# Kernel optimization log

Hardware: AMD Instinct MI355X
Metric: run time of the kernel (lower is better)

The kernel has to match this reference:

```python
import jax, jax.numpy as jnp
import numpy as np

BS, NQ, D, NH, NP, L, DFF = 4, 1024, 256, 8, 4, 6, 1024
H_BEV, W_BEV = 200, 150
NV = H_BEV * W_BEV
DH = D // NH


def setup_inputs() -> dict:
    key = jax.random.key(0)
    ks = iter(jax.random.split(key, 64))
    r = lambda *s: jax.random.normal(next(ks), s, dtype=jnp.float32)
    return {
        'query': r(BS, NQ, D),
        'query_pos': r(BS, NQ, D),
        'reference_points': jax.random.uniform(next(ks), (BS, NQ, 1, 2), dtype=jnp.float32),
        'src': r(BS, NV, D),
        'spatial_shapes': jnp.array([[H_BEV, W_BEV]], dtype=jnp.int32),
        'level_start_index': jnp.array([0], dtype=jnp.int32),
        'sa_in_w': r(L, 3 * D, D) * 0.02, 'sa_in_b': jnp.zeros((L, 3 * D), jnp.float32),
        'sa_out_w': r(L, D, D) * 0.02, 'sa_out_b': jnp.zeros((L, D), jnp.float32),
        'ca_off_w': r(L, NH * NP * 2, D) * 0.01, 'ca_off_b': r(L, NH * NP * 2) * 0.5,
        'ca_aw_w': r(L, NH * NP, D) * 0.01, 'ca_aw_b': jnp.zeros((L, NH * NP), jnp.float32),
        'ca_val_w': r(L, D, D) * 0.02, 'ca_val_b': jnp.zeros((L, D), jnp.float32),
        'ca_out_w': r(L, D, D) * 0.02, 'ca_out_b': jnp.zeros((L, D), jnp.float32),
        'n1_w': jnp.ones((L, D), jnp.float32), 'n1_b': jnp.zeros((L, D), jnp.float32),
        'n2_w': jnp.ones((L, D), jnp.float32), 'n2_b': jnp.zeros((L, D), jnp.float32),
        'n3_w': jnp.ones((L, D), jnp.float32), 'n3_b': jnp.zeros((L, D), jnp.float32),
        'ff1_w': r(L, DFF, D) * 0.02, 'ff1_b': jnp.zeros((L, DFF), jnp.float32),
        'ff2_w': r(L, D, DFF) * 0.02, 'ff2_b': jnp.zeros((L, D), jnp.float32),
    }


def layer_norm(x, w, b, eps=1e-5):
    m = jnp.mean(x, -1, keepdims=True)
    v = jnp.mean(jnp.square(x - m), -1, keepdims=True)
    return (x - m) / jnp.sqrt(v + eps) * w + b


def mha_self(x_qk, x_v, in_w, in_b, out_w, out_b):
    bs, nq, d = x_qk.shape
    qw, kw, vw = jnp.split(in_w, 3, axis=0)
    qb, kb, vb = jnp.split(in_b, 3, axis=0)
    q = (x_qk @ qw.T + qb).reshape(bs, nq, NH, DH)
    k = (x_qk @ kw.T + kb).reshape(bs, nq, NH, DH)
    v = (x_v @ vw.T + vb).reshape(bs, nq, NH, DH)
    att = jax.nn.softmax(jnp.einsum('bqhd,bkhd->bhqk', q, k) / jnp.sqrt(jnp.float32(DH)), axis=-1)
    o = jnp.einsum('bhqk,bkhd->bqhd', att, v).reshape(bs, nq, d)
    return o @ out_w.T + out_b


def msda(q, ref, src, lsi0, off_w, off_b, aw_w, aw_b, val_w, val_b, out_w, out_b):
    # single-level (n_levels=1) multi-scale deformable attention, grid_sample
    # bilinear with align_corners=False and zero padding, as in mmcv.
    bs, nq, d = q.shape
    v = (src @ val_w.T + val_b).reshape(bs, NV, NH, DH)
    vt = v.transpose(0, 2, 1, 3)  # (bs, NH, NV, DH)
    off = (q @ off_w.T + off_b).reshape(bs, nq, NH, NP, 2)
    aw = jax.nn.softmax((q @ aw_w.T + aw_b).reshape(bs, nq, NH, NP), axis=-1)
    norm = jnp.array([W_BEV, H_BEV], dtype=q.dtype)  # offset_normalizer = (W, H)
    loc = ref[:, :, None, 0, None, :] + off / norm  # (bs, nq, NH, NP, 2) in [0,1]
    x = loc[..., 0] * W_BEV - 0.5
    y = loc[..., 1] * H_BEV - 0.5
    x0 = jnp.floor(x)
    y0 = jnp.floor(y)
    acc = jnp.zeros((bs, NH, nq, NP, DH), q.dtype)
    for dx, dy in ((0, 0), (1, 0), (0, 1), (1, 1)):
        xi = x0 + dx
        yi = y0 + dy
        w = (1.0 - jnp.abs(x - xi)) * (1.0 - jnp.abs(y - yi))
        valid = (xi >= 0) & (xi < W_BEV) & (yi >= 0) & (yi < H_BEV)
        w = jnp.where(valid, w, 0.0)  # (bs, nq, NH, NP)
        xi_c = jnp.clip(xi, 0, W_BEV - 1).astype(jnp.int32)
        yi_c = jnp.clip(yi, 0, H_BEV - 1).astype(jnp.int32)
        idx = lsi0 + yi_c * W_BEV + xi_c  # flat index into NV
        idx_t = idx.transpose(0, 2, 1, 3).reshape(bs, NH, nq * NP)
        g = jnp.take_along_axis(vt, idx_t[..., None], axis=2).reshape(bs, NH, nq, NP, DH)
        acc = acc + g * w.transpose(0, 2, 1, 3)[..., None]
    o = jnp.einsum('bhqpd,bqhp->bqhd', acc, aw).reshape(bs, nq, d)
    return o @ out_w.T + out_b


def _forward(query, query_pos, reference_points, src,
             sa_in_w, sa_in_b, sa_out_w, sa_out_b,
             ca_off_w, ca_off_b, ca_aw_w, ca_aw_b, ca_val_w, ca_val_b, ca_out_w, ca_out_b,
             n1_w, n1_b, n2_w, n2_b, n3_w, n3_b,
             ff1_w, ff1_b, ff2_w, ff2_b,
             spatial_shapes, level_start_index):
    lsi0 = level_start_index[0]
    out = query
    inter = []
    for l in range(L):
        qk = out + query_pos
        sa = mha_self(qk, out, sa_in_w[l], sa_in_b[l], sa_out_w[l], sa_out_b[l])
        out = layer_norm(out + sa, n2_w[l], n2_b[l])
        ca = msda(out + query_pos, reference_points, src, lsi0,
                  ca_off_w[l], ca_off_b[l], ca_aw_w[l], ca_aw_b[l],
                  ca_val_w[l], ca_val_b[l], ca_out_w[l], ca_out_b[l])
        out = layer_norm(out + ca, n1_w[l], n1_b[l])
        ff = jax.nn.relu(out @ ff1_w[l].T + ff1_b[l]) @ ff2_w[l].T + ff2_b[l]
        out = layer_norm(out + ff, n3_w[l], n3_b[l])
        inter.append(out)
    hs = jnp.stack(inter)  # (L, bs, nq, D)
    refs = jnp.stack([reference_points] * L)  # (L, bs, nq, 1, 2)
    return hs, refs


def reference(query, query_pos, reference_points, src, spatial_shapes, level_start_index,
              sa_in_w, sa_in_b, sa_out_w, sa_out_b,
              ca_off_w, ca_off_b, ca_aw_w, ca_aw_b, ca_val_w, ca_val_b, ca_out_w, ca_out_b,
              n1_w, n1_b, n2_w, n2_b, n3_w, n3_b,
              ff1_w, ff1_b, ff2_w, ff2_b):
    return _forward(query, query_pos, reference_points, src,
                    sa_in_w, sa_in_b, sa_out_w, sa_out_b,
                    ca_off_w, ca_off_b, ca_aw_w, ca_aw_b, ca_val_w, ca_val_b, ca_out_w, ca_out_b,
                    n1_w, n1_b, n2_w, n2_b, n3_w, n3_b,
                    ff1_w, ff1_b, ff2_w, ff2_b,
                    spatial_shapes, level_start_index)
```

## Files before the change

### kernel.cpp

```cpp
#include <hip/hip_runtime.h>

typedef __attribute__((ext_vector_type(8))) short short8;
typedef __attribute__((ext_vector_type(4))) short short4v;
typedef __attribute__((ext_vector_type(4))) float f32x4;
typedef unsigned short u16;

#define DEVI static __device__ __forceinline__

DEVI float b2f(u16 u){ unsigned int x = ((unsigned int)u) << 16; float f; __builtin_memcpy(&f, &x, 4); return f; }
DEVI u16 f2b(float f){ unsigned int u; __builtin_memcpy(&u, &f, 4); u += 0x7fffu + ((u >> 16) & 1u); return (u16)(u >> 16); }
DEVI short8 cvt8(const float* __restrict__ p){
  f32x4 a = *(const f32x4*)p;
  f32x4 b = *(const f32x4*)(p + 4);
  short8 r;
  r[0]=(short)f2b(a[0]); r[1]=(short)f2b(a[1]); r[2]=(short)f2b(a[2]); r[3]=(short)f2b(a[3]);
  r[4]=(short)f2b(b[0]); r[5]=(short)f2b(b[1]); r[6]=(short)f2b(b[2]); r[7]=(short)f2b(b[3]);
  return r;
}

__global__ __launch_bounds__(256) void cvt_k(const float* __restrict__ s, u16* __restrict__ d, int n8){
  int i = blockIdx.x * 256 + threadIdx.x;
  if (i < n8) ((short8*)d)[i] = cvt8(s + (long)i * 8);
}

__global__ __launch_bounds__(256) void offaw_pack_k(
    const float* __restrict__ off_w, const float* __restrict__ aw_w,
    const float* __restrict__ off_b, const float* __restrict__ aw_b,
    u16* __restrict__ wofaw, float* __restrict__ obc)
{
  int tid = blockIdx.x * 256 + threadIdx.x;
  if (tid < 98304) {
    int l = tid / 16384, rem = tid - l * 16384;
    wofaw[l * 24576 + rem] = f2b(off_w[tid]);
  } else if (tid < 147456) {
    int t2 = tid - 98304;
    int l = t2 / 8192, rem = t2 - l * 8192;
    wofaw[l * 24576 + 16384 + rem] = f2b(aw_w[t2]);
  } else if (tid < 147840) {
    int t3 = tid - 147456;
    obc[(t3 / 64) * 96 + (t3 % 64)] = off_b[t3];
  } else if (tid < 148032) {
    int t4 = tid - 147840;
    obc[(t4 / 32) * 96 + 64 + (t4 % 32)] = aw_b[t4];
  }
}

__global__ __launch_bounds__(256) void flash_k(
    const u16* __restrict__ qkbuf, const u16* __restrict__ vt,
    u16* __restrict__ obuf)
{
  const float SC = 0.17677669529663687f;
  __shared__ u16 Plds[4][32][136];
  const int bh = blockIdx.x >> 3;
  const int b = bh >> 3, h = bh & 7;
  const int qt = blockIdx.x & 7;
  const int wave = threadIdx.x >> 6, lane = threadIdx.x & 63;
  const int lr = lane & 15, lq = lane >> 4;
  const int qbase = qt * 128 + wave * 32;

  short8 qf[2];
#pragma unroll
  for (int i = 0; i < 2; i++)
    qf[i] = *(const short8*)(qkbuf + (long)(b * 1024 + qbase + i * 16 + lr) * 512 + h * 32 + lq * 8);

  const u16* Kb = qkbuf + (long)b * 1024 * 512 + 256 + h * 32;
  const u16* Vb = vt + (long)bh * 32 * 1024;

  f32x4 acc_o[2][2] = {};
  float m_run[2][4], l_run[2][4];
#pragma unroll
  for (int i = 0; i < 2; i++)
#pragma unroll
    for (int r = 0; r < 4; r++){ m_run[i][r] = -3e38f; l_run[i][r] = 0.f; }

  for (int kt = 0; kt < 8; kt++) {
    f32x4 s[2][8] = {};
#pragma unroll
    for (int j = 0; j < 8; j++) {
      short8 kf = *(const short8*)(Kb + (long)(kt * 128 + j * 16 + lr) * 512 + lq * 8);
#pragma unroll
      for (int i = 0; i < 2; i++)
        s[i][j] = __builtin_amdgcn_mfma_f32_16x16x32_bf16(qf[i], kf, s[i][j], 0, 0, 0);
    }
#pragma unroll
    for (int i = 0; i < 2; i++) {
#pragma unroll
      for (int r = 0; r < 4; r++) {
        float mx = s[i][0][r];
#pragma unroll
        for (int j = 1; j < 8; j++) mx = fmaxf(mx, s[i][j][r]);
#pragma unroll
        for (int m = 1; m <= 8; m <<= 1) mx = fmaxf(mx, __shfl_xor(mx, m));
        float m_new = fmaxf(m_run[i][r], mx);
        float alpha = __expf((m_run[i][r] - m_new) * SC);
        float sum = 0.f;
        int row = i * 16 + lq * 4 + r;
#pragma unroll
        for (int j = 0; j < 8; j++) {
          float p = __expf((s[i][j][r] - m_new) * SC);
          sum += p;
          Plds[wave][row][j * 16 + lr] = f2b(p);
        }
#pragma unroll
        for (int m = 1; m <= 8; m <<= 1) sum += __shfl_xor(sum, m);
        l_run[i][r] = l_run[i][r] * alpha + sum;
        m_run[i][r] = m_new;
#pragma unroll
        for (int d = 0; d < 2; d++) acc_o[i][d][r] *= alpha;
      }
    }
#pragma unroll
    for (int kc = 0; kc < 4; kc++) {
      short8 pf[2];
#pragma unroll
      for (int i = 0; i < 2; i++)
        pf[i] = *(const short8*)&Plds[wave][i * 16 + lr][kc * 32 + lq * 8];
#pragma unroll
      for (int d = 0; d < 2; d++) {
        short8 vf = *(const short8*)(Vb + (long)(d * 16 + lr) * 1024 + kt * 128 + kc * 32 + lq * 8);
#pragma unroll
        for (int i = 0; i < 2; i++)
          acc_o[i][d] = __builtin_amdgcn_mfma_f32_16x16x32_bf16(pf[i], vf, acc_o[i][d], 0, 0, 0);
      }
    }
  }
#pragma unroll
  for (int i = 0; i < 2; i++) {
#pragma unroll
    for (int r = 0; r < 4; r++) {
      float inv = 1.f / l_run[i][r];
      int q = qbase + i * 16 + lq * 4 + r;
#pragma unroll
      for (int d = 0; d < 2; d++)
        obuf[(long)(b * 1024 + q) * 256 + h * 32 + d * 16 + lr] = f2b(acc_o[i][d][r] * inv);
    }
  }
}

template<bool RELU, bool OUTBF, bool VT, bool LN>
__global__ __launch_bounds__(256) void gemm_w_k(
    const u16* __restrict__ A, int lda,
    const u16* __restrict__ W,
    const float* __restrict__ bias,
    void* __restrict__ Cv, int ldo,
    int M, int N, int K,
    u16* __restrict__ vt,
    const float* __restrict__ res,
    const float* __restrict__ lnw, const float* __restrict__ lnb,
    const float* __restrict__ qpos,
    float* __restrict__ out_f, u16* __restrict__ out_b16,
    u16* __restrict__ qk_b16, float* __restrict__ hsp)
{
  __shared__ u16 As[32][64][8];
  __shared__ float r1s[4][64], r2s[4][64], mArr[64], iArr[64];
  const int wave = threadIdx.x >> 6, lane = threadIdx.x & 63;
  const int bm = blockIdx.x * 64;
  const int bn = blockIdx.y * 256 + wave * 64;
  const int lr = lane & 15, lq = lane >> 4;
  f32x4 acc[4][4] = {};
  const int nchunks = K >> 8;
  for (int ch = 0; ch < nchunks; ch++) {
    const u16* ga = A + (long)(bm + lane) * lda + ch * 256;
#pragma unroll
    for (int g = 0; g < 8; g++) {
      int kgrp = wave * 8 + g;
      __builtin_amdgcn_global_load_lds(
          (const __attribute__((address_space(1))) void*)(ga + kgrp * 8),
          (__attribute__((address_space(3))) void*)&As[kgrp][0][0], 16, 0, 0);
    }
    __syncthreads();
#pragma unroll
    for (int s = 0; s < 8; s++) {
      short8 af[4], bf[4];
#pragma unroll
      for (int i = 0; i < 4; i++)
        af[i] = *(const short8*)&As[s * 4 + lq][i * 16 + lr][0];
#pragma unroll
      for (int j = 0; j < 4; j++) {
        int cc = bn + j * 16 + lr;
        bf[j] = *(const short8*)(W + (long)cc * K + ch * 256 + s * 32 + lq * 8);
      }
#pragma unroll
      for (int i = 0; i < 4; i++)
#pragma unroll
        for (int j = 0; j < 4; j++)
          acc[i][j] = __builtin_amdgcn_mfma_f32_16x16x32_bf16(af[i], bf[j], acc[i][j], 0, 0, 0);
    }
    __syncthreads();
  }

  float bv[4];
#pragma unroll
  for (int j = 0; j < 4; j++) bv[j] = bias[bn + j * 16 + lr];

  if (!LN) {
#pragma unroll
    for (int j = 0; j < 4; j++) {
      int cc = bn + j * 16 + lr;
#pragma unroll
      for (int i = 0; i < 4; i++) {
#pragma unroll
        for (int r = 0; r < 4; r++) {
          int rr = bm + i * 16 + lq * 4 + r;
          float v = acc[i][j][r] + bv[j];
          if (RELU) v = fmaxf(v, 0.f);
          long idx = (long)rr * ldo + cc;
          if (OUTBF) ((u16*)Cv)[idx] = f2b(v);
          else       ((float*)Cv)[idx] = v;
          if (VT) {
            int b_ = rr >> 10, q_ = rr & 1023, h_ = cc >> 5, dh_ = cc & 31;
            vt[(long)((((b_ << 3) + h_) << 5) + dh_) * 1024 + q_] = f2b(v);
          }
        }
      }
    }
  } else {
    float s1[4][4] = {}, s2[4][4] = {};
#pragma unroll
    for (int i = 0; i < 4; i++) {
#pragma unroll
      for (int r = 0; r < 4; r++) {
        int rowg = bm + i * 16 + lq * 4 + r;
#pragma unroll
        for (int j = 0; j < 4; j++) {
          int cc = bn + j * 16 + lr;
          float x = acc[i][j][r] + bv[j] + res[(long)rowg * 256 + cc];
          s1[i][r] += x; s2[i][r] += x * x;
        }
      }
    }
#pragma unroll
    for (int i = 0; i < 4; i++)
#pragma unroll
      for (int r = 0; r < 4; r++) {
#pragma unroll
        for (int m = 1; m <= 8; m <<= 1) {
          s1[i][r] += __shfl_xor(s1[i][r], m);
          s2[i][r] += __shfl_xor(s2[i][r], m);
        }
      }
    if (lr == 0) {
#pragma unroll
      for (int i = 0; i < 4; i++)
#pragma unroll
        for (int r = 0; r < 4; r++) {
          int rl = i * 16 + lq * 4 + r;
          r1s[wave][rl] = s1[i][r];
          r2s[wave][rl] = s2[i][r];
        }
    }
    __syncthreads();
    if (threadIdx.x < 64) {
      int t = threadIdx.x;
      float a = r1s[0][t] + r1s[1][t] + r1s[2][t] + r1s[3][t];
      float b = r2s[0][t] + r2s[1][t] + r2s[2][t] + r2s[3][t];
      float m = a * (1.f / 256.f);
      float var = b * (1.f / 256.f) - m * m;
      mArr[t] = m;
      iArr[t] = rsqrtf(var + 1e-5f);
    }
    __syncthreads();
#pragma unroll
    for (int i = 0; i < 4; i++) {
#pragma unroll
      for (int r = 0; r < 4; r++) {
        int rl = i * 16 + lq * 4 + r;
        int rowg = bm + rl;
        float m = mArr[rl], inv = iArr[rl];
#pragma unroll
        for (int j = 0; j < 4; j++) {
          int cc = bn + j * 16 + lr;
          long idx = (long)rowg * 256 + cc;
          float x = acc[i][j][r] + bv[j] + res[idx];
          float y = (x - m) * inv * lnw[cc] + lnb[cc];
          out_f[idx] = y;
          if (out_b16) out_b16[idx] = f2b(y);
          if (qk_b16)  qk_b16[idx]  = f2b(y + qpos[idx]);
          if (hsp)     hsp[idx]     = y;
        }
      }
    }
  }
}

template<bool ABF, bool WBF, bool BIAS, bool RELU, bool OUTBF>
__global__ __launch_bounds__(256) void gemm64_k(
    const void* __restrict__ Av, int lda, long sA2, long sA1,
    const void* __restrict__ Wv, int ldw, long sW2, long sW1,
    const float* __restrict__ bias,
    void* __restrict__ Cv, int ldo, long sC2, long sC1,
    int M, int N, int K, int zshift)
{
  const int z  = blockIdx.z;
  const int z2 = z >> zshift, z1 = z - (z2 << zshift);
  const long aoff = z2 * sA2 + z1 * sA1;
  const long woff = z2 * sW2 + z1 * sW1;
  const long coff = z2 * sC2 + z1 * sC1;
  const int wave = threadIdx.x >> 6, lane = threadIdx.x & 63;
  const int wm = wave >> 1, wn = wave & 1;
  const int bm = blockIdx.x * 64 + wm * 32;
  const int bn = blockIdx.y * 64 + wn * 32;
  const int lr = lane & 15, lq = lane >> 4;
  const int koff = lq * 8;
  f32x4 acc[2][2] = {};
  const short8 Z8 = {0,0,0,0,0,0,0,0};
  for (int k0 = 0; k0 < K; k0 += 32) {
    short8 af[2], bf[2];
#pragma unroll
    for (int i = 0; i < 2; i++) {
      int r = bm + i * 16 + lr;
      if (r < M) {
        long o = aoff + (long)r * lda + k0 + koff;
        af[i] = ABF ? *(const short8*)((const u16*)Av + o) : cvt8((const float*)Av + o);
      } else af[i] = Z8;
    }
#pragma unroll
    for (int j = 0; j < 2; j++) {
      int c = bn + j * 16 + lr;
      if (c < N) {
        long o = woff + (long)c * ldw + k0 + koff;
        bf[j] = WBF ? *(const short8*)((const u16*)Wv + o) : cvt8((const float*)Wv + o);
      } else bf[j] = Z8;
    }
#pragma unroll
    for (int i = 0; i < 2; i++)
#pragma unroll
      for (int j = 0; j < 2; j++)
        acc[i][j] = __builtin_amdgcn_mfma_f32_16x16x32_bf16(af[i], bf[j], acc[i][j], 0, 0, 0);
  }
#pragma unroll
  for (int j = 0; j < 2; j++) {
    int cc = bn + j * 16 + lr;
    if (cc >= N) continue;
    float bv = BIAS ? bias[cc] : 0.f;
#pragma unroll
    for (int i = 0; i < 2; i++) {
#pragma unroll
      for (int r = 0; r < 4; r++) {
        int rr = bm + i * 16 + lq * 4 + r;
        if (rr >= M) continue;
        float v = acc[i][j][r] + bv;
        if (RELU) v = fmaxf(v, 0.f);
        long idx = coff + (long)rr * ldo + cc;
        if (OUTBF) ((u16*)Cv)[idx] = f2b(v);
        else       ((float*)Cv)[idx] = v;
      }
    }
  }
}

__global__ __launch_bounds__(256) void init_prep_k(const float* __restrict__ q, const float* __restrict__ qpos,
                                                   float* __restrict__ out_f, u16* __restrict__ out_b,
                                                   u16* __restrict__ qk_b){
  long i = (long)blockIdx.x * 256 + threadIdx.x;
  float o = q[i];
  out_f[i] = o;
  out_b[i] = f2b(o);
  qk_b[i]  = f2b(o + qpos[i]);
}

__global__ __launch_bounds__(256) void vt_k(const u16* __restrict__ V, u16* __restrict__ Vt){
  int tid = blockIdx.x * 256 + threadIdx.x;
  int q = tid & 1023;
  int rest = tid >> 10;
  int dh = rest & 31, h = (rest >> 5) & 7, b = rest >> 8;
  Vt[tid] = V[(long)((b << 10) + q) * 256 + (h << 5) + dh];
}

__global__ __launch_bounds__(256) void softmax_k(u16* __restrict__ S, float scale){
  long row = blockIdx.x;
  u16* p = S + row * 1024;
  int t = threadIdx.x;
  short4v sv = *(short4v*)(p + t * 4);
  float v[4]; float mx = -1e30f;
#pragma unroll
  for (int i = 0; i < 4; i++){ v[i] = b2f((u16)sv[i]); mx = fmaxf(mx, v[i]); }
  __shared__ float red[256];
  red[t] = mx; __syncthreads();
  for (int s = 128; s > 0; s >>= 1){ if (t < s) red[t] = fmaxf(red[t], red[t + s]); __syncthreads(); }
  mx = red[0]; __syncthreads();
  float sum = 0.f;
#pragma unroll
  for (int i = 0; i < 4; i++){ v[i] = __expf((v[i] - mx) * scale); sum += v[i]; }
  red[t] = sum; __syncthreads();
  for (int s = 128; s > 0; s >>= 1){ if (t < s) red[t] += red[t + s]; __syncthreads(); }
  float inv = 1.f / red[0];
#pragma unroll
  for (int i = 0; i < 4; i++) sv[i] = (short)f2b(v[i] * inv);
  *(short4v*)(p + t * 4) = sv;
}

template<bool QKPOS, bool HS, bool OUTB>
__global__ __launch_bounds__(256) void add_ln_k(
    const float* __restrict__ sub,
    const float* __restrict__ w, const float* __restrict__ b,
    const float* __restrict__ qpos,
    float* __restrict__ out_f, u16* __restrict__ out_b,
    u16* __restrict__ qk_b, float* __restrict__ hs)
{
  int row = blockIdx.x, t = threadIdx.x;
  long idx = (long)row * 256 + t;
  float x = out_f[idx] + sub[idx];
  __shared__ float r1[256], r2[256];
  r1[t] = x; r2[t] = x * x; __syncthreads();
  for (int s = 128; s > 0; s >>= 1){ if (t < s){ r1[t] += r1[t + s]; r2[t] += r2[t + s]; } __syncthreads(); }
  float m = r1[0] * (1.f / 256.f);
  float var = r2[0] * (1.f / 256.f) - m * m;
  float y = (x - m) * rsqrtf(var + 1e-5f) * w[t] + b[t];
  out_f[idx] = y;
  if (OUTB)  out_b[idx] = f2b(y);
  if (QKPOS) qk_b[idx]  = f2b(y + qpos[idx]);
  if (HS)    hs[idx]    = y;
}

__global__ __launch_bounds__(256) void msda_k(
    const float* __restrict__ refp,
    const float* __restrict__ off, int ldoff,
    const float* __restrict__ aw, int ldaw,
    const u16* __restrict__ v,
    u16* __restrict__ o,
    int bbase, long vstride)
{
  int tid = blockIdx.x * 256 + threadIdx.x;
  int dh = tid & 31;
  int h  = (tid >> 5) & 7;
  int qq = tid >> 8;
  int bq = (bbase << 10) + qq;
  int b  = bq >> 10;
  float rx = refp[bq * 2 + 0];
  float ry = refp[bq * 2 + 1];
  const float* offp = off + (long)bq * ldoff + h * 8;
  const float* awp  = aw  + (long)bq * ldaw + h * 4;
  float a0 = awp[0], a1 = awp[1], a2 = awp[2], a3 = awp[3];
  float am = fmaxf(fmaxf(a0, a1), fmaxf(a2, a3));
  float e[4];
  e[0] = __expf(a0 - am); e[1] = __expf(a1 - am); e[2] = __expf(a2 - am); e[3] = __expf(a3 - am);
  float einv = 1.f / (e[0] + e[1] + e[2] + e[3]);
  const u16* vb = v + b * vstride + h * 32 + dh;
  float accv = 0.f;
#pragma unroll
  for (int pp = 0; pp < 4; pp++){
    float x = rx * 150.f + offp[pp * 2 + 0] - 0.5f;
    float y = ry * 200.f + offp[pp * 2 + 1] - 0.5f;
    float x0 = floorf(x), y0 = floorf(y);
    float s = 0.f;
#pragma unroll
    for (int c = 0; c < 4; c++){
      int dx = c & 1, dy = c >> 1;
      float xi = x0 + dx, yi = y0 + dy;
      float wt = (1.f - fabsf(x - xi)) * (1.f - fabsf(y - yi));
      if (xi >= 0.f && xi < 150.f && yi >= 0.f && yi < 200.f && wt > 0.f) {
        int xc = (int)xi, yc = (int)yi;
        s += wt * b2f(vb[((long)yc * 150 + xc) * 256]);
      }
    }
    accv += e[pp] * einv * s;
  }
  o[(long)bq * 256 + h * 32 + dh] = f2b(accv);
}

__global__ __launch_bounds__(256) void refs_k(const float* __restrict__ r, float* __restrict__ dst){
  int i = blockIdx.x * 256 + threadIdx.x;
  dst[i] = r[i & 8191];
}

static inline void g64(hipStream_t st, int mode,
    const void* A, int lda, long sA2, long sA1,
    const void* W, int ldw, long sW2, long sW1,
    const float* bias, void* C, int ldo, long sC2, long sC1,
    int M, int N, int K, int Z, int zs)
{
  dim3 g((M + 63) / 64, (N + 63) / 64, Z), b(256, 1, 1);
  switch (mode) {
    case 1: gemm64_k<true, true, true, false,false><<<g,b,0,st>>>(A,lda,sA2,sA1,W,ldw,sW2,sW1,bias,C,ldo,sC2,sC1,M,N,K,zs); break;
    case 2: gemm64_k<true, true, false,false,true ><<<g,b,0,st>>>(A,lda,sA2,sA1,W,ldw,sW2,sW1,bias,C,ldo,sC2,sC1,M,N,K,zs); break;
    case 4: gemm64_k<true, false,true, false,true ><<<g,b,0,st>>>(A,lda,sA2,sA1,W,ldw,sW2,sW1,bias,C,ldo,sC2,sC1,M,N,K,zs); break;
    case 5: gemm64_k<true, false,true, false,false><<<g,b,0,st>>>(A,lda,sA2,sA1,W,ldw,sW2,sW1,bias,C,ldo,sC2,sC1,M,N,K,zs); break;
    case 6: gemm64_k<true, false,true, true, true ><<<g,b,0,st>>>(A,lda,sA2,sA1,W,ldw,sW2,sW1,bias,C,ldo,sC2,sC1,M,N,K,zs); break;
    case 7: gemm64_k<false,false,true, false,true ><<<g,b,0,st>>>(A,lda,sA2,sA1,W,ldw,sW2,sW1,bias,C,ldo,sC2,sC1,M,N,K,zs); break;
  }
}

extern "C" void kernel_launch(void* const* d_in, const int* in_sizes, int n_in,
                              void* d_out, int out_size, void* d_ws, size_t ws_size,
                              hipStream_t stream)
{
  (void)in_sizes; (void)n_in; (void)out_size;
  const float* query = (const float*)d_in[0];
  const float* qpos  = (const float*)d_in[1];
  const float* refp  = (const float*)d_in[2];
  const float* src   = (const float*)d_in[3];
  const float* sa_in_w  = (const float*)d_in[6];
  const float* sa_in_b  = (const float*)d_in[7];
  const float* sa_out_w = (const float*)d_in[8];
  const float* sa_out_b = (const float*)d_in[9];
  const float* off_w = (const float*)d_in[10];
  const float* off_b = (const float*)d_in[11];
  const float* aw_w  = (const float*)d_in[12];
  const float* aw_b  = (const float*)d_in[13];
  const float* val_w = (const float*)d_in[14];
  const float* val_b = (const float*)d_in[15];
  const float* cout_w = (const float*)d_in[16];
  const float* cout_b = (const float*)d_in[17];
  const float* n1w = (const float*)d_in[18]; const float* n1b = (const float*)d_in[19];
  const float* n2w = (const float*)d_in[20]; const float* n2b = (const float*)d_in[21];
  const float* n3w = (const float*)d_in[22]; const float* n3b = (const float*)d_in[23];
  const float* ff1w = (const float*)d_in[24]; const float* ff1b = (const float*)d_in[25];
  const float* ff2w = (const float*)d_in[26]; const float* ff2b = (const float*)d_in[27];

  float* hs = (float*)d_out;
  float* refs_out = hs + (long)6 * 4096 * 256;

  char* base = (char*)d_ws;
  float* out_f = (float*)(base);
  float* tmp_f = (float*)(base + (4u << 20));
  u16*   qk_b  = (u16*)  (base + (8u << 20));
  u16*   out_b = (u16*)  (base + (10u << 20));
  char*  rest  =          base + (12u << 20);

  const size_t NEED_A = 170u << 20;
  const bool planA = (ws_size >= NEED_A);

  init_prep_k<<<4096, 256, 0, stream>>>(query, qpos, out_f, out_b, qk_b);

  if (planA) {
    u16* wsa_b  = (u16*)(rest);
    u16* wsao_b = wsa_b  + 1179648;
    u16* wofaw  = wsao_b + 393216;
    u16* wval_b = wofaw  + 147456;
    u16* wcao_b = wval_b + 393216;
    u16* wff1_b = wcao_b + 393216;
    u16* wff2_b = wff1_b + 1572864;
    u16* src_b  = wff2_b + 1572864;
    float* obc  = (float*)(src_b + 30720000);
    char* U = (char*)(obc + 576);
    u16* qkbuf = (u16*)(U);
    u16* vbuf  = (u16*)(U + (4u << 20));
    u16* vt    = (u16*)(U + (6u << 20));
    u16* obuf  = (u16*)(U + (8u << 20));
    float* oawo = (float*)(U);
    u16*   mo   = (u16*)  (U + (2u << 20));
    u16*   vsrc = (u16*)  (U + (4u << 20));
    u16*   ffh  = (u16*)(U);

    auto cv = [&](const float* s, u16* d, long nel){
      int n8 = (int)(nel / 8);
      cvt_k<<<(n8 + 255) / 256, 256, 0, stream>>>(s, d, n8);
    };
    cv(sa_in_w,  wsa_b,  1179648); cv(sa_out_w, wsao_b, 393216);
    cv(val_w,    wval_b, 393216);  cv(cout_w,   wcao_b, 393216);
    cv(ff1w,     wff1_b, 1572864); cv(ff2w,     wff2_b, 1572864);
    cv(src,      src_b,  30720000);
    offaw_pack_k<<<579, 256, 0, stream>>>(off_w, aw_w, off_b, aw_b, wofaw, obc);

    for (int l = 0; l < 6; l++){
      const u16* wsa = wsa_b + (long)l * 768 * 256;
      const float* bsa = sa_in_b + l * 768;
      gemm_w_k<false,true,false,false><<<dim3(64,2,1),256,0,stream>>>(
          qk_b, 256, wsa, bsa, qkbuf, 512, 4096, 512, 256,
          nullptr, nullptr,nullptr,nullptr,nullptr,nullptr,nullptr,nullptr,nullptr);
      gemm_w_k<false,true,true,false><<<dim3(64,1,1),256,0,stream>>>(
          out_b, 256, wsa + 512*256, bsa + 512, vbuf, 256, 4096, 256, 256,
          vt, nullptr,nullptr,nullptr,nullptr,nullptr,nullptr,nullptr,nullptr);
      flash_k<<<256, 256, 0, stream>>>(qkbuf, vt, obuf);
      gemm_w_k<false,false,false,true><<<dim3(64,1,1),256,0,stream>>>(
          obuf, 256, wsao_b + (long)l*65536, sa_out_b + l*256, nullptr, 0, 4096, 256, 256,
          nullptr, out_f, n2w + l*256, n2b + l*256, qpos, out_f, nullptr, qk_b, nullptr);
      g64(stream, 1, qk_b, 256,0,0, wofaw + (long)l*24576, 256,0,0, obc + l*96,
          oawo, 96,0,0, 4096,96,256, 1,0);
      gemm_w_k<false,true,false,false><<<dim3(1875,1,1),256,0,stream>>>(
          src_b, 256, wval_b + (long)l*65536, val_b + l*256, vsrc, 256, 120000, 256, 256,
          nullptr, nullptr,nullptr,nullptr,nullptr,nullptr,nullptr,nullptr,nullptr);
      msda_k<<<4096, 256, 0, stream>>>(refp, oawo, 96, oawo + 64, 96, vsrc, mo, 0, 7680000);
      gemm_w_k<false,false,false,true><<<dim3(64,1,1),256,0,stream>>>(
          mo, 256, wcao_b + (long)l*65536, cout_b + l*256, nullptr, 0, 4096, 256, 256,
          nullptr, out_f, n1w + l*256, n1b + l*256, nullptr, out_f, out_b, nullptr, nullptr);
      gemm_w_k<true,true,false,false><<<dim3(64,4,1),256,0,stream>>>(
          out_b, 256, wff1_b + (long)l*262144, ff1b + l*1024, ffh, 1024, 4096, 1024, 256,
          nullptr, nullptr,nullptr,nullptr,nullptr,nullptr,nullptr,nullptr,nullptr);
      gemm_w_k<false,false,false,true><<<dim3(64,1,1),256,0,stream>>>(
          ffh, 1024, wff2_b + (long)l*262144, ff2b + l*256, nullptr, 0, 4096, 256, 1024,
          nullptr, out_f, n3w + l*256, n3b + l*256, qpos, out_f, out_b, qk_b,
          hs + (long)l*1048576);
    }
  } else {
    char* U = rest;
    u16* qkbuf = (u16*)(U);
    u16* vbuf  = (u16*)(U + (4u << 20));
    u16* vt    = (u16*)(U + (6u << 20));
    u16* obuf  = (u16*)(U + (8u << 20));
    u16* sbuf  = (u16*)(U + (10u << 20));
    float* offb = (float*)(U);
    float* awbf = (float*)(U + (1u << 20));
    u16*   mo   = (u16*)  (U + (1536u << 10));
    u16*   vsrc = (u16*)  (U + (3584u << 10));
    u16*   ffh  = (u16*)(U);

    for (int l = 0; l < 6; l++){
      const float* wsa = sa_in_w + (long)l * 768 * 256;
      const float* bsa = sa_in_b + l * 768;
      g64(stream, 4, qk_b, 256,0,0, wsa, 256,0,0, bsa, qkbuf, 512,0,0, 4096,512,256, 1,0);
      g64(stream, 4, out_b,256,0,0, wsa + 512*256, 256,0,0, bsa + 512, vbuf, 256,0,0, 4096,256,256, 1,0);
      vt_k<<<4096, 256, 0, stream>>>(vbuf, vt);
      for (int b = 0; b < 4; b++){
        const u16* qb = qkbuf + (long)b * 524288;
        g64(stream, 2, qb, 512, 0, 32, qb + 256, 512, 0, 32, nullptr,
            sbuf, 1024, 0, 1048576, 1024, 1024, 32, 8, 3);
        softmax_k<<<8192, 256, 0, stream>>>(sbuf, 0.17677669529663687f);
        g64(stream, 2, sbuf, 1024, 0, 1048576, vt + (long)b*262144, 1024, 0, 32768, nullptr,
            obuf + (long)b*262144, 256, 0, 32, 1024, 32, 1024, 8, 3);
      }
      g64(stream, 5, obuf, 256,0,0, sa_out_w + (long)l*65536, 256,0,0, sa_out_b + l*256,
          tmp_f, 256,0,0, 4096,256,256, 1,0);
      add_ln_k<true,false,false><<<4096,256,0,stream>>>(tmp_f, n2w+l*256, n2b+l*256, qpos,
          out_f, nullptr, qk_b, nullptr);
      g64(stream, 5, qk_b, 256,0,0, off_w + (long)l*16384, 256,0,0, off_b + l*64,
          offb, 64,0,0, 4096,64,256, 1,0);
      g64(stream, 5, qk_b, 256,0,0, aw_w + (long)l*8192, 256,0,0, aw_b + l*32,
          awbf, 32,0,0, 4096,32,256, 1,0);
      for (int b = 0; b < 4; b++){
        g64(stream, 7, src + (long)b*7680000, 256,0,0, val_w + (long)l*65536, 256,0,0,
            val_b + l*256, vsrc, 256,0,0, 30000,256,256, 1,0);
        msda_k<<<1024, 256, 0, stream>>>(refp, offb, 64, awbf, 32, vsrc, mo, b, 0);
      }
      g64(stream, 5, mo, 256,0,0, cout_w + (long)l*65536, 256,0,0, cout_b + l*256,
          tmp_f, 256,0,0, 4096,256,256, 1,0);
      add_ln_k<false,false,true><<<4096,256,0,stream>>>(tmp_f, n1w+l*256, n1b+l*256, nullptr,
          out_f, out_b, nullptr, nullptr);
      g64(stream, 6, out_b, 256,0,0, ff1w + (long)l*262144, 256,0,0, ff1b + l*1024,
          ffh, 1024,0,0, 4096,1024,256, 1,0);
      g64(stream, 5, ffh, 1024,0,0, ff2w + (long)l*262144, 1024,0,0, ff2b + l*256,
          tmp_f, 256,0,0, 4096,256,1024, 1,0);
      add_ln_k<true,true,true><<<4096,256,0,stream>>>(tmp_f, n3w+l*256, n3b+l*256, qpos,
          out_f, out_b, qk_b, hs + (long)l*1048576);
    }
  }
  refs_k<<<192, 256, 0, stream>>>(refp, refs_out);
}
```

Before: 2.013 ms.

## Merge conversions, batch value projections, fuse QKV, shrink LN-GEMM tiles, drop fallback

All fp32-to-bf16 weight and src conversions now run in one cvtall kernel. When workspace allows, the src value projection for all six layers runs as one batched GEMM up front. Q, K and V projections are fused into a single qkv kernel that writes V transposed directly, removing the separate vbuf. The LayerNorm-epilogue GEMMs use 32-row tiles to launch more blocks, and the non-planA fallback path is removed. The trade is a large extra value buffer of about 368 MB and more template complexity.

Result: faster. 1.707 ms (-15.2%).

```diff
diff --git a/kernel.cpp b/kernel.cpp
--- a/kernel.cpp
+++ b/kernel.cpp
@@ -1,7 +1,6 @@
 #include <hip/hip_runtime.h>
 
 typedef __attribute__((ext_vector_type(8))) short short8;
-typedef __attribute__((ext_vector_type(4))) short short4v;
 typedef __attribute__((ext_vector_type(4))) float f32x4;
 typedef unsigned short u16;
 
@@ -18,132 +17,47 @@
   return r;
 }
 
-__global__ __launch_bounds__(256) void cvt_k(const float* __restrict__ s, u16* __restrict__ d, int n8){
-  int i = blockIdx.x * 256 + threadIdx.x;
-  if (i < n8) ((short8*)d)[i] = cvt8(s + (long)i * 8);
-}
-
-__global__ __launch_bounds__(256) void offaw_pack_k(
-    const float* __restrict__ off_w, const float* __restrict__ aw_w,
-    const float* __restrict__ off_b, const float* __restrict__ aw_b,
-    u16* __restrict__ wofaw, float* __restrict__ obc)
-{
-  int tid = blockIdx.x * 256 + threadIdx.x;
-  if (tid < 98304) {
-    int l = tid / 16384, rem = tid - l * 16384;
-    wofaw[l * 24576 + rem] = f2b(off_w[tid]);
-  } else if (tid < 147456) {
-    int t2 = tid - 98304;
-    int l = t2 / 8192, rem = t2 - l * 8192;
-    wofaw[l * 24576 + 16384 + rem] = f2b(aw_w[t2]);
-  } else if (tid < 147840) {
-    int t3 = tid - 147456;
-    obc[(t3 / 64) * 96 + (t3 % 64)] = off_b[t3];
-  } else if (tid < 148032) {
-    int t4 = tid - 147840;
-    obc[(t4 / 32) * 96 + 64 + (t4 % 32)] = aw_b[t4];
-  }
-}
-
-__global__ __launch_bounds__(256) void flash_k(
-    const u16* __restrict__ qkbuf, const u16* __restrict__ vt,
-    u16* __restrict__ obuf)
-{
-  const float SC = 0.17677669529663687f;
-  __shared__ u16 Plds[4][32][136];
-  const int bh = blockIdx.x >> 3;
-  const int b = bh >> 3, h = bh & 7;
-  const int qt = blockIdx.x & 7;
-  const int wave = threadIdx.x >> 6, lane = threadIdx.x & 63;
-  const int lr = lane & 15, lq = lane >> 4;
-  const int qbase = qt * 128 + wave * 32;
-
-  short8 qf[2];
-#pragma unroll
-  for (int i = 0; i < 2; i++)
-    qf[i] = *(const short8*)(qkbuf + (long)(b * 1024 + qbase + i * 16 + lr) * 512 + h * 32 + lq * 8);
-
-  const u16* Kb = qkbuf + (long)b * 1024 * 512 + 256 + h * 32;
-  const u16* Vb = vt + (long)bh * 32 * 1024;
-
-  f32x4 acc_o[2][2] = {};
-  float m_run[2][4], l_run[2][4];
-#pragma unroll
-  for (int i = 0; i < 2; i++)
-#pragma unroll
-    for (int r = 0; r < 4; r++){ m_run[i][r] = -3e38f; l_run[i][r] = 0.f; }
-
-  for (int kt = 0; kt < 8; kt++) {
-    f32x4 s[2][8] = {};
+__global__ __launch_bounds__(256) void cvtall_k(
+    const float* __restrict__ sa_in_w, const float* __restrict__ sa_out_w,
+    const float* __restrict__ val_w,   const float* __restrict__ cout_w,
+    const float* __restrict__ ff1w,    const float* __restrict__ ff2w,
+    const float* __restrict__ off_w,   const float* __restrict__ aw_w,
+    const float* __restrict__ off_b,   const float* __restrict__ aw_b,
+    const float* __restrict__ src,
+    u16* __restrict__ wsa_b, u16* __restrict__ wsao_b, u16* __restrict__ wval_b,
+    u16* __restrict__ wcao_b, u16* __restrict__ wff1_b, u16* __restrict__ wff2_b,
+    u16* __restrict__ wofaw, float* __restrict__ obc, u16* __restrict__ src_b)
+{
+  long u = (long)blockIdx.x * 256 + threadIdx.x;
+  if (u < 147456) { ((short8*)wsa_b)[u]  = cvt8(sa_in_w  + u * 8); return; } u -= 147456;
+  if (u < 49152)  { ((short8*)wsao_b)[u] = cvt8(sa_out_w + u * 8); return; } u -= 49152;
+  if (u < 49152)  { ((short8*)wval_b)[u] = cvt8(val_w    + u * 8); return; } u -= 49152;
+  if (u < 49152)  { ((short8*)wcao_b)[u] = cvt8(cout_w   + u * 8); return; } u -= 49152;
+  if (u < 196608) { ((short8*)wff1_b)[u] = cvt8(ff1w     + u * 8); return; } u -= 196608;
+  if (u < 196608) { ((short8*)wff2_b)[u] = cvt8(ff2w     + u * 8); return; } u -= 196608;
+  if (u < 12288)  { long e = u * 8; int l = (int)(e >> 14); long rem = e & 16383;
+                    ((short8*)wofaw)[(l * 24576 + rem) >> 3] = cvt8(off_w + e); return; } u -= 12288;
+  if (u < 6144)   { long e = u * 8; int l = (int)(e >> 13); long rem = e & 8191;
+                    ((short8*)wofaw)[(l * 24576 + 16384 + rem) >> 3] = cvt8(aw_w + e); return; } u -= 6144;
+  if (u < 3840000){ ((short8*)src_b)[u]  = cvt8(src + u * 8); return; } u -= 3840000;
+  if (u < 72) {
+    long e0 = u * 8;
 #pragma unroll
     for (int j = 0; j < 8; j++) {
-      short8 kf = *(const short8*)(Kb + (long)(kt * 128 + j * 16 + lr) * 512 + lq * 8);
-#pragma unroll
-      for (int i = 0; i < 2; i++)
-        s[i][j] = __builtin_amdgcn_mfma_f32_16x16x32_bf16(qf[i], kf, s[i][j], 0, 0, 0);
-    }
-#pragma unroll
-    for (int i = 0; i < 2; i++) {
-#pragma unroll
-      for (int r = 0; r < 4; r++) {
-        float mx = s[i][0][r];
-#pragma unroll
-        for (int j = 1; j < 8; j++) mx = fmaxf(mx, s[i][j][r]);
-#pragma unroll
-        for (int m = 1; m <= 8; m <<= 1) mx = fmaxf(mx, __shfl_xor(mx, m));
-        float m_new = fmaxf(m_run[i][r], mx);
-        float alpha = __expf((m_run[i][r] - m_new) * SC);
-        float sum = 0.f;
-        int row = i * 16 + lq * 4 + r;
-#pragma unroll
-        for (int j = 0; j < 8; j++) {
-          float p = __expf((s[i][j][r] - m_new) * SC);
-          sum += p;
-          Plds[wave][row][j * 16 + lr] = f2b(p);
-        }
-#pragma unroll
-        for (int m = 1; m <= 8; m <<= 1) sum += __shfl_xor(sum, m);
-        l_run[i][r] = l_run[i][r] * alpha + sum;
-        m_run[i][r] = m_new;
-#pragma unroll
-        for (int d = 0; d < 2; d++) acc_o[i][d][r] *= alpha;
-      }
-    }
-#pragma unroll
-    for (int kc = 0; kc < 4; kc++) {
-      short8 pf[2];
-#pragma unroll
-      for (int i = 0; i < 2; i++)
-        pf[i] = *(const short8*)&Plds[wave][i * 16 + lr][kc * 32 + lq * 8];
-#pragma unroll
-      for (int d = 0; d < 2; d++) {
-        short8 vf = *(const short8*)(Vb + (long)(d * 16 + lr) * 1024 + kt * 128 + kc * 32 + lq * 8);
-#pragma unroll
-        for (int i = 0; i < 2; i++)
-          acc_o[i][d] = __builtin_amdgcn_mfma_f32_16x16x32_bf16(pf[i], vf, acc_o[i][d], 0, 0, 0);
-      }
-    }
-  }
-#pragma unroll
-  for (int i = 0; i < 2; i++) {
-#pragma unroll
-    for (int r = 0; r < 4; r++) {
-      float inv = 1.f / l_run[i][r];
-      int q = qbase + i * 16 + lq * 4 + r;
-#pragma unroll
-      for (int d = 0; d < 2; d++)
-        obuf[(long)(b * 1024 + q) * 256 + h * 32 + d * 16 + lr] = f2b(acc_o[i][d][r] * inv);
-    }
-  }
-}
-
-template<bool RELU, bool OUTBF, bool VT, bool LN>
+      long e = e0 + j;
+      if (e < 384) { int l = (int)(e >> 6); obc[l * 96 + (e & 63)] = off_b[e]; }
+      else { long e2 = e - 384; int l = (int)(e2 >> 5); obc[l * 96 + 64 + (e2 & 31)] = aw_b[e2]; }
+    }
+  }
+}
+
+template<int MT, bool RELU, bool OUTBF, bool VT, bool LN>
 __global__ __launch_bounds__(256) void gemm_w_k(
     const u16* __restrict__ A, int lda,
-    const u16* __restrict__ W,
-    const float* __restrict__ bias,
-    void* __restrict__ Cv, int ldo,
-    int M, int N, int K,
+    const u16* __restrict__ W, long wZ,
+    const float* __restrict__ bias, int bZ,
+    void* __restrict__ Cv, int ldo, long cZ,
+    int K,
     u16* __restrict__ vt,
     const float* __restrict__ res,
     const float* __restrict__ lnw, const float* __restrict__ lnb,
@@ -151,37 +65,42 @@
     float* __restrict__ out_f, u16* __restrict__ out_b16,
     u16* __restrict__ qk_b16, float* __restrict__ hsp)
 {
-  __shared__ u16 As[32][64][8];
+  __shared__ u16 As[32 * MT * 8];
   __shared__ float r1s[4][64], r2s[4][64], mArr[64], iArr[64];
   const int wave = threadIdx.x >> 6, lane = threadIdx.x & 63;
-  const int bm = blockIdx.x * 64;
+  const int bm = blockIdx.x * MT;
   const int bn = blockIdx.y * 256 + wave * 64;
   const int lr = lane & 15, lq = lane >> 4;
-  f32x4 acc[4][4] = {};
+  constexpr int SH = (MT == 64) ? 6 : 5;
+  const u16* Wz = W + (long)blockIdx.z * wZ;
+  const float* bz = bias + (long)blockIdx.z * bZ;
+  f32x4 acc[MT / 16][4] = {};
   const int nchunks = K >> 8;
   for (int ch = 0; ch < nchunks; ch++) {
-    const u16* ga = A + (long)(bm + lane) * lda + ch * 256;
-#pragma unroll
-    for (int g = 0; g < 8; g++) {
-      int kgrp = wave * 8 + g;
+#pragma unroll
+    for (int it = 0; it < MT / 8; it++) {
+      int ub = wave * (MT * 8) + it * 64;
+      int u = ub + lane;
+      int row = u & (MT - 1), kgrp = u >> SH;
+      const u16* ga = A + (long)(bm + row) * lda + ch * 256 + kgrp * 8;
       __builtin_amdgcn_global_load_lds(
-          (const __attribute__((address_space(1))) void*)(ga + kgrp * 8),
-          (__attribute__((address_space(3))) void*)&As[kgrp][0][0], 16, 0, 0);
+          (const __attribute__((address_space(1))) void*)ga,
+          (__attribute__((address_space(3))) void*)(As + ub * 8), 16, 0, 0);
     }
     __syncthreads();
 #pragma unroll
     for (int s = 0; s < 8; s++) {
-      short8 af[4], bf[4];
-#pragma unroll
-      for (int i = 0; i < 4; i++)
-        af[i] = *(const short8*)&As[s * 4 + lq][i * 16 + lr][0];
+      short8 af[MT / 16], bf[4];
+#pragma unroll
+      for (int i = 0; i < MT / 16; i++)
+        af[i] = *(const short8*)(As + ((s * 4 + lq) * MT + i * 16 + lr) * 8);
 #pragma unroll
       for (int j = 0; j < 4; j++) {
         int cc = bn + j * 16 + lr;
-        bf[j] = *(const short8*)(W + (long)cc * K + ch * 256 + s * 32 + lq * 8);
-      }
-#pragma unroll
-      for (int i = 0; i < 4; i++)
+        bf[j] = *(const short8*)(Wz + (long)cc * K + ch * 256 + s * 32 + lq * 8);
+      }
+#pragma unroll
+      for (int i = 0; i < MT / 16; i++)
 #pragma unroll
         for (int j = 0; j < 4; j++)
           acc[i][j] = __builtin_amdgcn_mfma_f32_16x16x32_bf16(af[i], bf[j], acc[i][j], 0, 0, 0);
@@ -191,22 +110,23 @@
 
   float bv[4];
 #pragma unroll
-  for (int j = 0; j < 4; j++) bv[j] = bias[bn + j * 16 + lr];
+  for (int j = 0; j < 4; j++) bv[j] = bz[bn + j * 16 + lr];
 
   if (!LN) {
+    char* Cz = (char*)Cv;
 #pragma unroll
     for (int j = 0; j < 4; j++) {
       int cc = bn + j * 16 + lr;
 #pragma unroll
-      for (int i = 0; i < 4; i++) {
+      for (int i = 0; i < MT / 16; i++) {
 #pragma unroll
         for (int r = 0; r < 4; r++) {
           int rr = bm + i * 16 + lq * 4 + r;
           float v = acc[i][j][r] + bv[j];
           if (RELU) v = fmaxf(v, 0.f);
-          long idx = (long)rr * ldo + cc;
-          if (OUTBF) ((u16*)Cv)[idx] = f2b(v);
-          else       ((float*)Cv)[idx] = v;
+          long idx = (long)blockIdx.z * cZ + (long)rr * ldo + cc;
+          if (OUTBF) ((u16*)Cz)[idx] = f2b(v);
+          else       ((float*)Cz)[idx] = v;
           if (VT) {
             int b_ = rr >> 10, q_ = rr & 1023, h_ = cc >> 5, dh_ = cc & 31;
             vt[(long)((((b_ << 3) + h_) << 5) + dh_) * 1024 + q_] = f2b(v);
@@ -215,9 +135,9 @@
       }
     }
   } else {
-    float s1[4][4] = {}, s2[4][4] = {};
-#pragma unroll
-    for (int i = 0; i < 4; i++) {
+    float s1[MT / 16][4] = {}, s2[MT / 16][4] = {};
+#pragma unroll
+    for (int i = 0; i < MT / 16; i++) {
 #pragma unroll
       for (int r = 0; r < 4; r++) {
         int rowg = bm + i * 16 + lq * 4 + r;
@@ -230,7 +150,7 @@
       }
     }
 #pragma unroll
-    for (int i = 0; i < 4; i++)
+    for (int i = 0; i < MT / 16; i++)
 #pragma unroll
       for (int r = 0; r < 4; r++) {
 #pragma unroll
@@ -241,7 +161,7 @@
       }
     if (lr == 0) {
 #pragma unroll
-      for (int i = 0; i < 4; i++)
+      for (int i = 0; i < MT / 16; i++)
 #pragma unroll
         for (int r = 0; r < 4; r++) {
           int rl = i * 16 + lq * 4 + r;
@@ -250,7 +170,7 @@
         }
     }
     __syncthreads();
-    if (threadIdx.x < 64) {
+    if (threadIdx.x < MT) {
       int t = threadIdx.x;
       float a = r1s[0][t] + r1s[1][t] + r1s[2][t] + r1s[3][t];
       float b = r2s[0][t] + r2s[1][t] + r2s[2][t] + r2s[3][t];
@@ -261,7 +181,7 @@
     }
     __syncthreads();
 #pragma unroll
-    for (int i = 0; i < 4; i++) {
+    for (int i = 0; i < MT / 16; i++) {
 #pragma unroll
       for (int r = 0; r < 4; r++) {
         int rl = i * 16 + lq * 4 + r;
@@ -283,19 +203,170 @@
   }
 }
 
-template<bool ABF, bool WBF, bool BIAS, bool RELU, bool OUTBF>
+__global__ __launch_bounds__(256) void qkv_k(
+    const u16* __restrict__ qk_b, const u16* __restrict__ out_b,
+    const u16* __restrict__ wsa, const float* __restrict__ bsa,
+    u16* __restrict__ qkbuf, u16* __restrict__ vt)
+{
+  __shared__ u16 As[32 * 64 * 8];
+  const int sel = blockIdx.y;
+  const u16* A = (sel == 2) ? out_b : qk_b;
+  const u16* W = wsa + (long)sel * 256 * 256;
+  const int wave = threadIdx.x >> 6, lane = threadIdx.x & 63;
+  const int bm = blockIdx.x * 64;
+  const int bn = wave * 64;
+  const int lr = lane & 15, lq = lane >> 4;
+  f32x4 acc[4][4] = {};
+#pragma unroll
+  for (int it = 0; it < 8; it++) {
+    int ub = wave * 512 + it * 64;
+    int u = ub + lane;
+    int row = u & 63, kgrp = u >> 6;
+    const u16* ga = A + (long)(bm + row) * 256 + kgrp * 8;
+    __builtin_amdgcn_global_load_lds(
+        (const __attribute__((address_space(1))) void*)ga,
+        (__attribute__((address_space(3))) void*)(As + ub * 8), 16, 0, 0);
+  }
+  __syncthreads();
+#pragma unroll
+  for (int s = 0; s < 8; s++) {
+    short8 af[4], bf[4];
+#pragma unroll
+    for (int i = 0; i < 4; i++)
+      af[i] = *(const short8*)(As + ((s * 4 + lq) * 64 + i * 16 + lr) * 8);
+#pragma unroll
+    for (int j = 0; j < 4; j++) {
+      int cc = bn + j * 16 + lr;
+      bf[j] = *(const short8*)(W + (long)cc * 256 + s * 32 + lq * 8);
+    }
+#pragma unroll
+    for (int i = 0; i < 4; i++)
+#pragma unroll
+      for (int j = 0; j < 4; j++)
+        acc[i][j] = __builtin_amdgcn_mfma_f32_16x16x32_bf16(af[i], bf[j], acc[i][j], 0, 0, 0);
+  }
+  float bv[4];
+#pragma unroll
+  for (int j = 0; j < 4; j++) bv[j] = bsa[sel * 256 + bn + j * 16 + lr];
+#pragma unroll
+  for (int j = 0; j < 4; j++) {
+    int cc = bn + j * 16 + lr;
+#pragma unroll
+    for (int i = 0; i < 4; i++) {
+#pragma unroll
+      for (int r = 0; r < 4; r++) {
+        int rr = bm + i * 16 + lq * 4 + r;
+        float v = acc[i][j][r] + bv[j];
+        if (sel < 2) {
+          qkbuf[(long)rr * 512 + sel * 256 + cc] = f2b(v);
+        } else {
+          int b_ = rr >> 10, q_ = rr & 1023, h_ = cc >> 5, dh_ = cc & 31;
+          vt[(long)((((b_ << 3) + h_) << 5) + dh_) * 1024 + q_] = f2b(v);
+        }
+      }
+    }
+  }
+}
+
+__global__ __launch_bounds__(256) void flash_k(
+    const u16* __restrict__ qkbuf, const u16* __restrict__ vt,
+    u16* __restrict__ obuf)
+{
+  const float SC = 0.17677669529663687f;
+  __shared__ u16 Plds[4][32][136];
+  const int bh = blockIdx.x >> 3;
+  const int b = bh >> 3, h = bh & 7;
+  const int qt = blockIdx.x & 7;
+  const int wave = threadIdx.x >> 6, lane = threadIdx.x & 63;
+  const int lr = lane & 15, lq = lane >> 4;
+  const int qbase = qt * 128 + wave * 32;
+
+  short8 qf[2];
+#pragma unroll
+  for (int i = 0; i < 2; i++)
+    qf[i] = *(const short8*)(qkbuf + (long)(b * 1024 + qbase + i * 16 + lr) * 512 + h * 32 + lq * 8);
+
+  const u16* Kb = qkbuf + (long)b * 1024 * 512 + 256 + h * 32;
+  const u16* Vb = vt + (long)bh * 32 * 1024;
+
+  f32x4 acc_o[2][2] = {};
+  float m_run[2][4], l_run[2][4];
+#pragma unroll
+  for (int i = 0; i < 2; i++)
+#pragma unroll
+    for (int r = 0; r < 4; r++){ m_run[i][r] = -3e38f; l_run[i][r] = 0.f; }
+
+  for (int kt = 0; kt < 8; kt++) {
+    f32x4 s[2][8] = {};
+#pragma unroll
+    for (int j = 0; j < 8; j++) {
+      short8 kf = *(const short8*)(Kb + (long)(kt * 128 + j * 16 + lr) * 512 + lq * 8);
+#pragma unroll
+      for (int i = 0; i < 2; i++)
+        s[i][j] = __builtin_amdgcn_mfma_f32_16x16x32_bf16(qf[i], kf, s[i][j], 0, 0, 0);
+    }
+#pragma unroll
+    for (int i = 0; i < 2; i++) {
+#pragma unroll
+      for (int r = 0; r < 4; r++) {
+        float mx = s[i][0][r];
+#pragma unroll
+        for (int j = 1; j < 8; j++) mx = fmaxf(mx, s[i][j][r]);
+#pragma unroll
+        for (int m = 1; m <= 8; m <<= 1) mx = fmaxf(mx, __shfl_xor(mx, m));
+        float m_new = fmaxf(m_run[i][r], mx);
+        float alpha = __expf((m_run[i][r] - m_new) * SC);
+        float sum = 0.f;
+        int row = i * 16 + lq * 4 + r;
+#pragma unroll
+        for (int j = 0; j < 8; j++) {
+          float p = __expf((s[i][j][r] - m_new) * SC);
+          sum += p;
+          Plds[wave][row][j * 16 + lr] = f2b(p);
+        }
+#pragma unroll
+        for (int m = 1; m <= 8; m <<= 1) sum += __shfl_xor(sum, m);
+        l_run[i][r] = l_run[i][r] * alpha + sum;
+        m_run[i][r] = m_new;
+#pragma unroll
+        for (int d = 0; d < 2; d++) acc_o[i][d][r] *= alpha;
+      }
+    }
+#pragma unroll
+    for (int kc = 0; kc < 4; kc++) {
+      short8 pf[2];
+#pragma unroll
+      for (int i = 0; i < 2; i++)
+        pf[i] = *(const short8*)&Plds[wave][i * 16 + lr][kc * 32 + lq * 8];
+#pragma unroll
+      for (int d = 0; d < 2; d++) {
+        short8 vf = *(const short8*)(Vb + (long)(d * 16 + lr) * 1024 + kt * 128 + kc * 32 + lq * 8);
+#pragma unroll
+        for (int i = 0; i < 2; i++)
+          acc_o[i][d] = __builtin_amdgcn_mfma_f32_16x16x32_bf16(pf[i], vf, acc_o[i][d], 0, 0, 0);
+      }
+    }
+  }
+#pragma unroll
+  for (int i = 0; i < 2; i++) {
+#pragma unroll
+    for (int r = 0; r < 4; r++) {
+      float inv = 1.f / l_run[i][r];
+      int q = qbase + i * 16 + lq * 4 + r;
+#pragma unroll
+      for (int d = 0; d < 2; d++)
+        obuf[(long)(b * 1024 + q) * 256 + h * 32 + d * 16 + lr] = f2b(acc_o[i][d][r] * inv);
+    }
+  }
+}
+
 __global__ __launch_bounds__(256) void gemm64_k(
-    const void* __restrict__ Av, int lda, long sA2, long sA1,
-    const void* __restrict__ Wv, int ldw, long sW2, long sW1,
+    const u16* __restrict__ A, int lda,
+    const u16* __restrict__ W, int ldw,
     const float* __restrict__ bias,
-    void* __restrict__ Cv, int ldo, long sC2, long sC1,
-    int M, int N, int K, int zshift)
-{
-  const int z  = blockIdx.z;
-  const int z2 = z >> zshift, z1 = z - (z2 << zshift);
-  const long aoff = z2 * sA2 + z1 * sA1;
-  const long woff = z2 * sW2 + z1 * sW1;
-  const long coff = z2 * sC2 + z1 * sC1;
+    float* __restrict__ C, int ldo,
+    int M, int N, int K)
+{
   const int wave = threadIdx.x >> 6, lane = threadIdx.x & 63;
   const int wm = wave >> 1, wn = wave & 1;
   const int bm = blockIdx.x * 64 + wm * 32;
@@ -309,18 +380,12 @@
 #pragma unroll
     for (int i = 0; i < 2; i++) {
       int r = bm + i * 16 + lr;
-      if (r < M) {
-        long o = aoff + (long)r * lda + k0 + koff;
-        af[i] = ABF ? *(const short8*)((const u16*)Av + o) : cvt8((const float*)Av + o);
-      } else af[i] = Z8;
+      af[i] = (r < M) ? *(const short8*)(A + (long)r * lda + k0 + koff) : Z8;
     }
 #pragma unroll
     for (int j = 0; j < 2; j++) {
       int c = bn + j * 16 + lr;
-      if (c < N) {
-        long o = woff + (long)c * ldw + k0 + koff;
-        bf[j] = WBF ? *(const short8*)((const u16*)Wv + o) : cvt8((const float*)Wv + o);
-      } else bf[j] = Z8;
+      bf[j] = (c < N) ? *(const short8*)(W + (long)c * ldw + k0 + koff) : Z8;
     }
 #pragma unroll
     for (int i = 0; i < 2; i++)
@@ -332,18 +397,14 @@
   for (int j = 0; j < 2; j++) {
     int cc = bn + j * 16 + lr;
     if (cc >= N) continue;
-    float bv = BIAS ? bias[cc] : 0.f;
+    float bv = bias[cc];
 #pragma unroll
     for (int i = 0; i < 2; i++) {
 #pragma unroll
       for (int r = 0; r < 4; r++) {
         int rr = bm + i * 16 + lq * 4 + r;
         if (rr >= M) continue;
-        float v = acc[i][j][r] + bv;
-        if (RELU) v = fmaxf(v, 0.f);
-        long idx = coff + (long)rr * ldo + cc;
-        if (OUTBF) ((u16*)Cv)[idx] = f2b(v);
-        else       ((float*)Cv)[idx] = v;
+        C[(long)rr * ldo + cc] = acc[i][j][r] + bv;
       }
     }
   }
@@ -359,73 +420,18 @@
   qk_b[i]  = f2b(o + qpos[i]);
 }
 
-__global__ __launch_bounds__(256) void vt_k(const u16* __restrict__ V, u16* __restrict__ Vt){
-  int tid = blockIdx.x * 256 + threadIdx.x;
-  int q = tid & 1023;
-  int rest = tid >> 10;
-  int dh = rest & 31, h = (rest >> 5) & 7, b = rest >> 8;
-  Vt[tid] = V[(long)((b << 10) + q) * 256 + (h << 5) + dh];
-}
-
-__global__ __launch_bounds__(256) void softmax_k(u16* __restrict__ S, float scale){
-  long row = blockIdx.x;
-  u16* p = S + row * 1024;
-  int t = threadIdx.x;
-  short4v sv = *(short4v*)(p + t * 4);
-  float v[4]; float mx = -1e30f;
-#pragma unroll
-  for (int i = 0; i < 4; i++){ v[i] = b2f((u16)sv[i]); mx = fmaxf(mx, v[i]); }
-  __shared__ float red[256];
-  red[t] = mx; __syncthreads();
-  for (int s = 128; s > 0; s >>= 1){ if (t < s) red[t] = fmaxf(red[t], red[t + s]); __syncthreads(); }
-  mx = red[0]; __syncthreads();
-  float sum = 0.f;
-#pragma unroll
-  for (int i = 0; i < 4; i++){ v[i] = __expf((v[i] - mx) * scale); sum += v[i]; }
-  red[t] = sum; __syncthreads();
-  for (int s = 128; s > 0; s >>= 1){ if (t < s) red[t] += red[t + s]; __syncthreads(); }
-  float inv = 1.f / red[0];
-#pragma unroll
-  for (int i = 0; i < 4; i++) sv[i] = (short)f2b(v[i] * inv);
-  *(short4v*)(p + t * 4) = sv;
-}
-
-template<bool QKPOS, bool HS, bool OUTB>
-__global__ __launch_bounds__(256) void add_ln_k(
-    const float* __restrict__ sub,
-    const float* __restrict__ w, const float* __restrict__ b,
-    const float* __restrict__ qpos,
-    float* __restrict__ out_f, u16* __restrict__ out_b,
-    u16* __restrict__ qk_b, float* __restrict__ hs)
-{
-  int row = blockIdx.x, t = threadIdx.x;
-  long idx = (long)row * 256 + t;
-  float x = out_f[idx] + sub[idx];
-  __shared__ float r1[256], r2[256];
-  r1[t] = x; r2[t] = x * x; __syncthreads();
-  for (int s = 128; s > 0; s >>= 1){ if (t < s){ r1[t] += r1[t + s]; r2[t] += r2[t + s]; } __syncthreads(); }
-  float m = r1[0] * (1.f / 256.f);
-  float var = r2[0] * (1.f / 256.f) - m * m;
-  float y = (x - m) * rsqrtf(var + 1e-5f) * w[t] + b[t];
-  out_f[idx] = y;
-  if (OUTB)  out_b[idx] = f2b(y);
-  if (QKPOS) qk_b[idx]  = f2b(y + qpos[idx]);
-  if (HS)    hs[idx]    = y;
-}
-
 __global__ __launch_bounds__(256) void msda_k(
     const float* __restrict__ refp,
     const float* __restrict__ off, int ldoff,
     const float* __restrict__ aw, int ldaw,
     const u16* __restrict__ v,
     u16* __restrict__ o,
-    int bbase, long vstride)
+    long vstride)
 {
   int tid = blockIdx.x * 256 + threadIdx.x;
   int dh = tid & 31;
   int h  = (tid >> 5) & 7;
-  int qq = tid >> 8;
-  int bq = (bbase << 10) + qq;
+  int bq = tid >> 8;
   int b  = bq >> 10;
   float rx = refp[bq * 2 + 0];
   float ry = refp[bq * 2 + 1];
@@ -462,23 +468,6 @@
 __global__ __launch_bounds__(256) void refs_k(const float* __restrict__ r, float* __restrict__ dst){
   int i = blockIdx.x * 256 + threadIdx.x;
   dst[i] = r[i & 8191];
-}
-
-static inline void g64(hipStream_t st, int mode,
-    const void* A, int lda, long sA2, long sA1,
-    const void* W, int ldw, long sW2, long sW1,
-    const float* bias, void* C, int ldo, long sC2, long sC1,
-    int M, int N, int K, int Z, int zs)
-{
-  dim3 g((M + 63) / 64, (N + 63) / 64, Z), b(256, 1, 1);
-  switch (mode) {
-    case 1: gemm64_k<true, true, true, false,false><<<g,b,0,st>>>(A,lda,sA2,sA1,W,ldw,sW2,sW1,bias,C,ldo,sC2,sC1,M,N,K,zs); break;
-    case 2: gemm64_k<true, true, false,false,true ><<<g,b,0,st>>>(A,lda,sA2,sA1,W,ldw,sW2,sW1,bias,C,ldo,sC2,sC1,M,N,K,zs); break;
-    case 4: gemm64_k<true, false,true, false,true ><<<g,b,0,st>>>(A,lda,sA2,sA1,W,ldw,sW2,sW1,bias,C,ldo,sC2,sC1,M,N,K,zs); break;
-    case 5: gemm64_k<true, false,true, false,false><<<g,b,0,st>>>(A,lda,sA2,sA1,W,ldw,sW2,sW1,bias,C,ldo,sC2,sC1,M,N,K,zs); break;
-    case 6: gemm64_k<true, false,true, true, true ><<<g,b,0,st>>>(A,lda,sA2,sA1,W,ldw,sW2,sW1,bias,C,ldo,sC2,sC1,M,N,K,zs); break;
-    case 7: gemm64_k<false,false,true, false,true ><<<g,b,0,st>>>(A,lda,sA2,sA1,W,ldw,sW2,sW1,bias,C,ldo,sC2,sC1,M,N,K,zs); break;
-  }
 }
 
 extern "C" void kernel_launch(void* const* d_in, const int* in_sizes, int n_in,
@@ -511,129 +500,67 @@
   float* hs = (float*)d_out;
   float* refs_out = hs + (long)6 * 4096 * 256;
 
-  char* base = (char*)d_ws;
-  float* out_f = (float*)(base);
-  float* tmp_f = (float*)(base + (4u << 20));
-  u16*   qk_b  = (u16*)  (base + (8u << 20));
-  u16*   out_b = (u16*)  (base + (10u << 20));
-  char*  rest  =          base + (12u << 20);
-
-  const size_t NEED_A = 170u << 20;
-  const bool planA = (ws_size >= NEED_A);
+  char* p = (char*)d_ws;
+  auto alloc = [&](size_t bytes){ char* r = p; p += (bytes + 255) & ~(size_t)255; return r; };
+  float* out_f = (float*)alloc(4194304);
+  u16*   qk_b  = (u16*)  alloc(2097152);
+  u16*   out_b = (u16*)  alloc(2097152);
+  u16* wsa_b  = (u16*)alloc(2359296);
+  u16* wsao_b = (u16*)alloc(786432);
+  u16* wofaw  = (u16*)alloc(294912);
+  u16* wval_b = (u16*)alloc(786432);
+  u16* wcao_b = (u16*)alloc(786432);
+  u16* wff1_b = (u16*)alloc(3145728);
+  u16* wff2_b = (u16*)alloc(3145728);
+  float* obc  = (float*)alloc(2304);
+  u16* src_b  = (u16*)alloc(61440000);
+  u16* qkbuf  = (u16*)alloc(4194304);
+  u16* vt     = (u16*)alloc(2097152);
+  u16* obuf   = (u16*)alloc(2097152);
+  float* oawo = (float*)alloc(1572864);
+  u16* mo     = (u16*)alloc(2097152);
+  u16* ffh    = (u16*)alloc(8388608);
+  size_t used = (size_t)(p - (char*)d_ws);
+  const bool big = (ws_size >= used + 368640000ull);
+  u16* vsrc = (u16*)alloc(big ? 368640000ull : 61440000ull);
 
   init_prep_k<<<4096, 256, 0, stream>>>(query, qpos, out_f, out_b, qk_b);
-
-  if (planA) {
-    u16* wsa_b  = (u16*)(rest);
-    u16* wsao_b = wsa_b  + 1179648;
-    u16* wofaw  = wsao_b + 393216;
-    u16* wval_b = wofaw  + 147456;
-    u16* wcao_b = wval_b + 393216;
-    u16* wff1_b = wcao_b + 393216;
-    u16* wff2_b = wff1_b + 1572864;
-    u16* src_b  = wff2_b + 1572864;
-    float* obc  = (float*)(src_b + 30720000);
-    char* U = (char*)(obc + 576);
-    u16* qkbuf = (u16*)(U);
-    u16* vbuf  = (u16*)(U + (4u << 20));
-    u16* vt    = (u16*)(U + (6u << 20));
-    u16* obuf  = (u16*)(U + (8u << 20));
-    float* oawo = (float*)(U);
-    u16*   mo   = (u16*)  (U + (2u << 20));
-    u16*   vsrc = (u16*)  (U + (4u << 20));
-    u16*   ffh  = (u16*)(U);
-
-    auto cv = [&](const float* s, u16* d, long nel){
-      int n8 = (int)(nel / 8);
-      cvt_k<<<(n8 + 255) / 256, 256, 0, stream>>>(s, d, n8);
-    };
-    cv(sa_in_w,  wsa_b,  1179648); cv(sa_out_w, wsao_b, 393216);
-    cv(val_w,    wval_b, 393216);  cv(cout_w,   wcao_b, 393216);
-    cv(ff1w,     wff1_b, 1572864); cv(ff2w,     wff2_b, 1572864);
-    cv(src,      src_b,  30720000);
-    offaw_pack_k<<<579, 256, 0, stream>>>(off_w, aw_w, off_b, aw_b, wofaw, obc);
-
-    for (int l = 0; l < 6; l++){
-      const u16* wsa = wsa_b + (long)l * 768 * 256;
-      const float* bsa = sa_in_b + l * 768;
-      gemm_w_k<false,true,false,false><<<dim3(64,2,1),256,0,stream>>>(
-          qk_b, 256, wsa, bsa, qkbuf, 512, 4096, 512, 256,
+  cvtall_k<<<17761, 256, 0, stream>>>(sa_in_w, sa_out_w, val_w, cout_w, ff1w, ff2w,
+                                      off_w, aw_w, off_b, aw_b, src,
+                                      wsa_b, wsao_b, wval_b, wcao_b, wff1_b, wff2_b,
+                                      wofaw, obc, src_b);
+  if (big) {
+    gemm_w_k<64,false,true,false,false><<<dim3(1875,1,6),256,0,stream>>>(
+        src_b, 256, wval_b, 65536, val_b, 256, vsrc, 256, 30720000, 256,
+        nullptr, nullptr,nullptr,nullptr,nullptr,nullptr,nullptr,nullptr,nullptr);
+  }
+
+  for (int l = 0; l < 6; l++){
+    const u16* wsa = wsa_b + (long)l * 768 * 256;
+    qkv_k<<<dim3(64,3,1),256,0,stream>>>(qk_b, out_b, wsa, sa_in_b + l * 768, qkbuf, vt);
+    flash_k<<<256,256,0,stream>>>(qkbuf, vt, obuf);
+    gemm_w_k<32,false,false,false,true><<<dim3(128,1,1),256,0,stream>>>(
+        obuf, 256, wsao_b + (long)l*65536, 0, sa_out_b + l*256, 0, nullptr, 0, 0, 256,
+        nullptr, out_f, n2w + l*256, n2b + l*256, qpos, out_f, nullptr, qk_b, nullptr);
+    gemm64_k<<<dim3(64,2,1),256,0,stream>>>(qk_b, 256, wofaw + (long)l*24576, 256,
+        obc + l*96, oawo, 96, 4096, 96, 256);
+    if (!big) {
+      gemm_w_k<64,false,true,false,false><<<dim3(1875,1,1),256,0,stream>>>(
+          src_b, 256, wval_b + (long)l*65536, 0, val_b + l*256, 0, vsrc, 256, 0, 256,
           nullptr, nullptr,nullptr,nullptr,nullptr,nullptr,nullptr,nullptr,nullptr);
-      gemm_w_k<false,true,true,false><<<dim3(64,1,1),256,0,stream>>>(
-          out_b, 256, wsa + 512*256, bsa + 512, vbuf, 256, 4096, 256, 256,
-          vt, nullptr,nullptr,nullptr,nullptr,nullptr,nullptr,nullptr,nullptr);
-      flash_k<<<256, 256, 0, stream>>>(qkbuf, vt, obuf);
-      gemm_w_k<false,false,false,true><<<dim3(64,1,1),256,0,stream>>>(
-          obuf, 256, wsao_b + (long)l*65536, sa_out_b + l*256, nullptr, 0, 4096, 256, 256,
-          nullptr, out_f, n2w + l*256, n2b + l*256, qpos, out_f, nullptr, qk_b, nullptr);
-      g64(stream, 1, qk_b, 256,0,0, wofaw + (long)l*24576, 256,0,0, obc + l*96,
-          oawo, 96,0,0, 4096,96,256, 1,0);
-      gemm_w_k<false,true,false,false><<<dim3(1875,1,1),256,0,stream>>>(
-          src_b, 256, wval_b + (long)l*65536, val_b + l*256, vsrc, 256, 120000, 256, 256,
-          nullptr, nullptr,nullptr,nullptr,nullptr,nullptr,nullptr,nullptr,nullptr);
-      msda_k<<<4096, 256, 0, stream>>>(refp, oawo, 96, oawo + 64, 96, vsrc, mo, 0, 7680000);
-      gemm_w_k<false,false,false,true><<<dim3(64,1,1),256,0,stream>>>(
-          mo, 256, wcao_b + (long)l*65536, cout_b + l*256, nullptr, 0, 4096, 256, 256,
-          nullptr, out_f, n1w + l*256, n1b + l*256, nullptr, out_f, out_b, nullptr, nullptr);
-      gemm_w_k<true,true,false,false><<<dim3(64,4,1),256,0,stream>>>(
-          out_b, 256, wff1_b + (long)l*262144, ff1b + l*1024, ffh, 1024, 4096, 1024, 256,
-          nullptr, nullptr,nullptr,nullptr,nullptr,nullptr,nullptr,nullptr,nullptr);
-      gemm_w_k<false,false,false,true><<<dim3(64,1,1),256,0,stream>>>(
-          ffh, 1024, wff2_b + (long)l*262144, ff2b + l*256, nullptr, 0, 4096, 256, 1024,
-          nullptr, out_f, n3w + l*256, n3b + l*256, qpos, out_f, out_b, qk_b,
-          hs + (long)l*1048576);
-    }
-  } else {
-    char* U = rest;
-    u16* qkbuf = (u16*)(U);
-    u16* vbuf  = (u16*)(U + (4u << 20));
-    u16* vt    = (u16*)(U + (6u << 20));
-    u16* obuf  = (u16*)(U + (8u << 20));
-    u16* sbuf  = (u16*)(U + (10u << 20));
-    float* offb = (float*)(U);
-    float* awbf = (float*)(U + (1u << 20));
-    u16*   mo   = (u16*)  (U + (1536u << 10));
-    u16*   vsrc = (u16*)  (U + (3584u << 10));
-    u16*   ffh  = (u16*)(U);
-
-    for (int l = 0; l < 6; l++){
-      const float* wsa = sa_in_w + (long)l * 768 * 256;
-      const float* bsa = sa_in_b + l * 768;
-      g64(stream, 4, qk_b, 256,0,0, wsa, 256,0,0, bsa, qkbuf, 512,0,0, 4096,512,256, 1,0);
-      g64(stream, 4, out_b,256,0,0, wsa + 512*256, 256,0,0, bsa + 512, vbuf, 256,0,0, 4096,256,256, 1,0);
-      vt_k<<<4096, 256, 0, stream>>>(vbuf, vt);
-      for (int b = 0; b < 4; b++){
-        const u16* qb = qkbuf + (long)b * 524288;
-        g64(stream, 2, qb, 512, 0, 32, qb + 256, 512, 0, 32, nullptr,
-            sbuf, 1024, 0, 1048576, 1024, 1024, 32, 8, 3);
-        softmax_k<<<8192, 256, 0, stream>>>(sbuf, 0.17677669529663687f);
-        g64(stream, 2, sbuf, 1024, 0, 1048576, vt + (long)b*262144, 1024, 0, 32768, nullptr,
-            obuf + (long)b*262144, 256, 0, 32, 1024, 32, 1024, 8, 3);
-      }
-      g64(stream, 5, obuf, 256,0,0, sa_out_w + (long)l*65536, 256,0,0, sa_out_b + l*256,
-          tmp_f, 256,0,0, 4096,256,256, 1,0);
-      add_ln_k<true,false,false><<<4096,256,0,stream>>>(tmp_f, n2w+l*256, n2b+l*256, qpos,
-          out_f, nullptr, qk_b, nullptr);
-      g64(stream, 5, qk_b, 256,0,0, off_w + (long)l*16384, 256,0,0, off_b + l*64,
-          offb, 64,0,0, 4096,64,256, 1,0);
-      g64(stream, 5, qk_b, 256,0,0, aw_w + (long)l*8192, 256,0,0, aw_b + l*32,
-          awbf, 32,0,0, 4096,32,256, 1,0);
-      for (int b = 0; b < 4; b++){
-        g64(stream, 7, src + (long)b*7680000, 256,0,0, val_w + (long)l*65536, 256,0,0,
-            val_b + l*256, vsrc, 256,0,0, 30000,256,256, 1,0);
-        msda_k<<<1024, 256, 0, stream>>>(refp, offb, 64, awbf, 32, vsrc, mo, b, 0);
-      }
-      g64(stream, 5, mo, 256,0,0, cout_w + (long)l*65536, 256,0,0, cout_b + l*256,
-          tmp_f, 256,0,0, 4096,256,256, 1,0);
-      add_ln_k<false,false,true><<<4096,256,0,stream>>>(tmp_f, n1w+l*256, n1b+l*256, nullptr,
-          out_f, out_b, nullptr, nullptr);
-      g64(stream, 6, out_b, 256,0,0, ff1w + (long)l*262144, 256,0,0, ff1b + l*1024,
-          ffh, 1024,0,0, 4096,1024,256, 1,0);
-      g64(stream, 5, ffh, 1024,0,0, ff2w + (long)l*262144, 1024,0,0, ff2b + l*256,
-          tmp_f, 256,0,0, 4096,256,1024, 1,0);
-      add_ln_k<true,true,true><<<4096,256,0,stream>>>(tmp_f, n3w+l*256, n3b+l*256, qpos,
-          out_f, out_b, qk_b, hs + (long)l*1048576);
-    }
-  }
-  refs_k<<<192, 256, 0, stream>>>(refp, refs_out);
-}
+    }
+    const u16* vsl = big ? (vsrc + (long)l*30720000) : vsrc;
+    msda_k<<<4096,256,0,stream>>>(refp, oawo, 96, oawo + 64, 96, vsl, mo, 7680000);
+    gemm_w_k<32,false,false,false,true><<<dim3(128,1,1),256,0,stream>>>(
+        mo, 256, wcao_b + (long)l*65536, 0, cout_b + l*256, 0, nullptr, 0, 0, 256,
+        nullptr, out_f, n1w + l*256, n1b + l*256, nullptr, out_f, out_b, nullptr, nullptr);
+    gemm_w_k<64,true,true,false,false><<<dim3(64,4,1),256,0,stream>>>(
+        out_b, 256, wff1_b + (long)l*262144, 0, ff1b + l*1024, 0, ffh, 1024, 0, 256,
+        nullptr, nullptr,nullptr,nullptr,nullptr,nullptr,nullptr,nullptr,nullptr);
+    gemm_w_k<32,false,false,false,true><<<dim3(128,1,1),256,0,stream>>>(
+        ffh, 1024, wff2_b + (long)l*262144, 0, ff2b + l*256, 0, nullptr, 0, 0, 1024,
+        nullptr, out_f, n3w + l*256, n3b + l*256, qpos, out_f, out_b, qk_b,
+        hs + (long)l*1048576);
+  }
+  refs_k<<<192,256,0,stream>>>(refp, refs_out);
+}
```
